# Optimization experiments

Measured on AMD Instinct MI355X. Metric: run time of the kernel, lower is better.

The kernel has to match this reference:

```python
import math
import jax, jax.numpy as jnp
import numpy as np

B, S, D, H = 2, 2048, 1024, 16
DK = D // H


def setup_inputs() -> dict:
    key = jax.random.key(0)
    ks = jax.random.split(key, 12)
    scale = 1.0 / math.sqrt(D)
    inp = {
        "q": jax.random.normal(ks[0], (B, S, D), jnp.float32),
        "k": jax.random.normal(ks[1], (B, S, D), jnp.float32),
        "v": jax.random.normal(ks[2], (B, S, D), jnp.float32),
        # causal mask, broadcast over batch and heads (mask==0 -> -inf)
        "mask": jnp.tril(jnp.ones((S, S), jnp.int32))[None, None, :, :],
        "Wq": jax.random.normal(ks[3], (D, D), jnp.float32) * scale,
        "bq": jnp.zeros((D,), jnp.float32),
        "Wk": jax.random.normal(ks[4], (D, D), jnp.float32) * scale,
        "bk": jnp.zeros((D,), jnp.float32),
        "Wv": jax.random.normal(ks[5], (D, D), jnp.float32) * scale,
        "bv": jnp.zeros((D,), jnp.float32),
        "Wo": jax.random.normal(ks[6], (D, D), jnp.float32) * scale,
        "bo": jnp.zeros((D,), jnp.float32),
    }
    return inp


def reference(q, k, v, mask, Wq, bq, Wk, bk, Wv, bv, Wo, bo):
    def proj(x, W, b):
        # [B,S,D] -> [B,H,S,DK]
        return (x @ W + b).reshape(B, -1, H, DK).transpose(0, 2, 1, 3)

    Q = proj(q, Wq, bq)
    K = proj(k, Wk, bk)
    V = proj(v, Wv, bv)
    scores = jnp.einsum("bhqd,bhkd->bhqk", Q, K) / math.sqrt(DK)  # [B,H,S,S]
    scores = jnp.where(mask == 0, -jnp.inf, scores)
    attn = jax.nn.softmax(scores, axis=-1)  # dropout p=0.0 -> identity
    ctx = jnp.einsum("bhqk,bhkd->bhqd", attn, V)
    ctx = ctx.transpose(0, 2, 1, 3).reshape(B, -1, D)  # [B,S,D]
    return ctx @ Wo + bo
```

## Files before the change

kernel.cpp:

```cpp
#include <hip/hip_runtime.h>
#include <stdint.h>

#define BB 2
#define SS 2048
#define DD 1024
#define HH 16
#define DK 64

#define QSCALE 0.1803368801111204f
#define NEGS -1.0e30f

typedef short s16x8 __attribute__((ext_vector_type(8)));
typedef float f32x4 __attribute__((ext_vector_type(4)));
typedef unsigned short u16x4 __attribute__((ext_vector_type(4)));
typedef unsigned int u32x4 __attribute__((ext_vector_type(4)));

static __device__ __forceinline__ unsigned short f2bf(float f) {
  unsigned int u = __builtin_bit_cast(unsigned int, f);
  u = (u + 0x7fffu + ((u >> 16) & 1u)) >> 16;
  return (unsigned short)u;
}

static __device__ __forceinline__ unsigned int cvtpk(float lo, float hi) {
  unsigned int r;
  asm("v_cvt_pk_bf16_f32 %0, %1, %2" : "=v"(r) : "v"(lo), "v"(hi));
  return r;
}

static __device__ __forceinline__ f32x4 mfma16(s16x8 a, s16x8 b, f32x4 c) {
  return __builtin_amdgcn_mfma_f32_16x16x32_bf16(a, b, c, 0, 0, 0);
}

static __device__ __forceinline__ void gload_lds16(const void* g, void* l) {
  __builtin_amdgcn_global_load_lds(
      (const __attribute__((address_space(1))) unsigned int*)g,
      (__attribute__((address_space(3))) unsigned int*)l, 16, 0, 0);
}

__global__ __launch_bounds__(256) void cvt3_kernel(const float* __restrict__ q,
                                                   const float* __restrict__ k,
                                                   const float* __restrict__ v,
                                                   unsigned short* __restrict__ qb,
                                                   unsigned short* __restrict__ kb,
                                                   unsigned short* __restrict__ vb) {
  int sel = blockIdx.y;
  const float* in = (sel == 0) ? q : ((sel == 1) ? k : v);
  unsigned short* out = (sel == 0) ? qb : ((sel == 1) ? kb : vb);
  int i = blockIdx.x * 256 + threadIdx.x;
  f32x4 vv = ((const f32x4*)in)[i];
  u16x4 o;
  o.x = f2bf(vv.x); o.y = f2bf(vv.y); o.z = f2bf(vv.z); o.w = f2bf(vv.w);
  ((u16x4*)out)[i] = o;
}

__global__ __launch_bounds__(256) void transpose_w4_kernel(const float* __restrict__ Wq,
                                                           const float* __restrict__ Wk,
                                                           const float* __restrict__ Wv,
                                                           const float* __restrict__ Wo,
                                                           unsigned short* __restrict__ WTbase) {
  __shared__ float t[32][33];
  int z = blockIdx.z;
  const float* W = (z == 0) ? Wq : ((z == 1) ? Wk : ((z == 2) ? Wv : Wo));
  float scale = (z == 0) ? QSCALE : 1.0f;
  unsigned short* WT = WTbase + (size_t)z * DD * DD;
  int n0 = blockIdx.x * 32, k0 = blockIdx.y * 32;
  int tx = threadIdx.x, ty = threadIdx.y;
  for (int i = 0; i < 4; ++i)
    t[ty + 8 * i][tx] = W[(size_t)(k0 + ty + 8 * i) * DD + n0 + tx];
  __syncthreads();
  for (int i = 0; i < 4; ++i)
    WT[(size_t)(n0 + ty + 8 * i) * DD + k0 + tx] = f2bf(t[tx][ty + 8 * i] * scale);
}

__global__ __launch_bounds__(256) void transpose_v_kernel(const unsigned short* __restrict__ V,
                                                          unsigned short* __restrict__ VT) {
  __shared__ unsigned short t[32][33];
  int s0 = blockIdx.x * 32, d0 = blockIdx.y * 32, bh = blockIdx.z;
  int tx = threadIdx.x, ty = threadIdx.y;
  const unsigned short* Vb = V + (size_t)bh * SS * DK;
  unsigned short* Tb = VT + (size_t)bh * DK * SS;
  for (int i = 0; i < 4; ++i)
    t[ty + 8 * i][tx] = Vb[(size_t)(s0 + ty + 8 * i) * DK + d0 + tx];
  __syncthreads();
  for (int i = 0; i < 4; ++i)
    Tb[(size_t)(d0 + ty + 8 * i) * SS + s0 + tx] = t[tx][ty + 8 * i];
}

__global__ __launch_bounds__(256) void gemm_qkv_kernel(
    const unsigned short* __restrict__ qb, const unsigned short* __restrict__ kb,
    const unsigned short* __restrict__ vb, const unsigned short* __restrict__ WTbase,
    const float* __restrict__ bq, const float* __restrict__ bk,
    const float* __restrict__ bv, unsigned short* __restrict__ Qh,
    unsigned short* __restrict__ Kh, unsigned short* __restrict__ Vh) {
  const int K = DD;
  __shared__ __align__(16) unsigned short Alds[128 * 32];
  __shared__ __align__(16) unsigned short Blds[128 * 32];
  int tid = threadIdx.x;
  int lane = tid & 63, wave = tid >> 6;
  int g = lane >> 4, r16 = lane & 15;
  int seg = blockIdx.y >> 5;
  int m0 = (blockIdx.y & 31) * 128, n0 = blockIdx.x * 128;
  int wm = (wave >> 1) * 64, wn = (wave & 1) * 64;

  const unsigned short* A = (seg == 0) ? qb : ((seg == 1) ? kb : vb);
  const unsigned short* BT = WTbase + (size_t)seg * DD * DD;
  const float* bias = (seg == 0) ? bq : ((seg == 1) ? bk : bv);
  unsigned short* outh = (seg == 0) ? Qh : ((seg == 1) ? Kh : Vh);
  float bsc = (seg == 0) ? QSCALE : 1.0f;

  f32x4 acc[4][4] = {};

  int c0 = tid, c1 = tid + 256;
  int arow0 = c0 >> 2, arow1 = c1 >> 2;
  int as0 = (c0 & 3) ^ ((arow0 >> 1) & 3);
  int as1 = (c1 & 3) ^ ((arow1 >> 1) & 3);

  for (int k0 = 0; k0 < K; k0 += 32) {
    __syncthreads();
    gload_lds16((const char*)(A + (size_t)(m0 + arow0) * K + k0) + as0 * 16,
                (char*)Alds + wave * 1024);
    gload_lds16((const char*)(A + (size_t)(m0 + arow1) * K + k0) + as1 * 16,
                (char*)Alds + wave * 1024 + 4096);
    gload_lds16((const char*)(BT + (size_t)(n0 + arow0) * K + k0) + as0 * 16,
                (char*)Blds + wave * 1024);
    gload_lds16((const char*)(BT + (size_t)(n0 + arow1) * K + k0) + as1 * 16,
                (char*)Blds + wave * 1024 + 4096);
    __syncthreads();

    s16x8 af[4], bfr[4];
#pragma unroll
    for (int mt = 0; mt < 4; ++mt) {
      int row = wm + mt * 16 + r16;
      int ch = g ^ ((row >> 1) & 3);
      af[mt] = *(const s16x8*)((const char*)Alds + row * 64 + ch * 16);
    }
#pragma unroll
    for (int nt = 0; nt < 4; ++nt) {
      int row = wn + nt * 16 + r16;
      int ch = g ^ ((row >> 1) & 3);
      bfr[nt] = *(const s16x8*)((const char*)Blds + row * 64 + ch * 16);
    }
#pragma unroll
    for (int mt = 0; mt < 4; ++mt)
#pragma unroll
      for (int nt = 0; nt < 4; ++nt)
        acc[mt][nt] = mfma16(af[mt], bfr[nt], acc[mt][nt]);
  }

#pragma unroll
  for (int nt = 0; nt < 4; ++nt) {
    int col = n0 + wn + nt * 16 + r16;
    int h = col >> 6, dk = col & (DK - 1);
    float bvv = bias[col] * bsc;
#pragma unroll
    for (int mt = 0; mt < 4; ++mt) {
#pragma unroll
      for (int rr = 0; rr < 4; ++rr) {
        int rowg = m0 + wm + mt * 16 + g * 4 + rr;
        int bb = rowg >> 11, s = rowg & (SS - 1);
        float val = acc[mt][nt][rr] + bvv;
        outh[(((size_t)bb * HH + h) * SS + s) * DK + dk] = f2bf(val);
      }
    }
  }
}

__global__ __launch_bounds__(256) void gemm_out_kernel(const unsigned short* __restrict__ A,
                                                       const unsigned short* __restrict__ BT,
                                                       const float* __restrict__ bias,
                                                       float* __restrict__ out) {
  const int K = DD;
  __shared__ __align__(16) unsigned short Alds[128 * 32];
  __shared__ __align__(16) unsigned short Blds[64 * 32];
  int tid = threadIdx.x;
  int lane = tid & 63, wave = tid >> 6;
  int g = lane >> 4, r16 = lane & 15;
  int m0 = blockIdx.y * 128, n0 = blockIdx.x * 64;
  int wm = (wave >> 1) * 64, wn = (wave & 1) * 32;

  f32x4 acc[4][2] = {};

  int c0 = tid, c1 = tid + 256;
  int arow0 = c0 >> 2, arow1 = c1 >> 2;
  int as0 = (c0 & 3) ^ ((arow0 >> 1) & 3);
  int as1 = (c1 & 3) ^ ((arow1 >> 1) & 3);

  for (int k0 = 0; k0 < K; k0 += 32) {
    __syncthreads();
    gload_lds16((const char*)(A + (size_t)(m0 + arow0) * K + k0) + as0 * 16,
                (char*)Alds + wave * 1024);
    gload_lds16((const char*)(A + (size_t)(m0 + arow1) * K + k0) + as1 * 16,
                (char*)Alds + wave * 1024 + 4096);
    gload_lds16((const char*)(BT + (size_t)(n0 + arow0) * K + k0) + as0 * 16,
                (char*)Blds + wave * 1024);
    __syncthreads();

    s16x8 af[4], bfr[2];
#pragma unroll
    for (int mt = 0; mt < 4; ++mt) {
      int row = wm + mt * 16 + r16;
      int ch = g ^ ((row >> 1) & 3);
      af[mt] = *(const s16x8*)((const char*)Alds + row * 64 + ch * 16);
    }
#pragma unroll
    for (int nt = 0; nt < 2; ++nt) {
      int row = wn + nt * 16 + r16;
      int ch = g ^ ((row >> 1) & 3);
      bfr[nt] = *(const s16x8*)((const char*)Blds + row * 64 + ch * 16);
    }
#pragma unroll
    for (int mt = 0; mt < 4; ++mt)
#pragma unroll
      for (int nt = 0; nt < 2; ++nt)
        acc[mt][nt] = mfma16(af[mt], bfr[nt], acc[mt][nt]);
  }

#pragma unroll
  for (int nt = 0; nt < 2; ++nt) {
    int col = n0 + wn + nt * 16 + r16;
    float bvv = bias[col];
#pragma unroll
    for (int mt = 0; mt < 4; ++mt) {
#pragma unroll
      for (int rr = 0; rr < 4; ++rr) {
        int rowg = m0 + wm + mt * 16 + g * 4 + rr;
        out[(size_t)rowg * DD + col] = acc[mt][nt][rr] + bvv;
      }
    }
  }
}

__global__ __launch_bounds__(256) void attn_kernel(const unsigned short* __restrict__ Qh,
                                                   const unsigned short* __restrict__ Kh,
                                                   const unsigned short* __restrict__ VhT,
                                                   unsigned short* __restrict__ ctx) {
  __shared__ __align__(16) unsigned short Klds[2][64 * 64];
  __shared__ __align__(16) unsigned short Vlds[2][64 * 64];

  int tid = threadIdx.x;
  int lane = tid & 63, wave = tid >> 6;
  int g = lane >> 4, r16 = lane & 15;
  int pid = blockIdx.x;
  int bh = blockIdx.y;

  const int NTQ = SS / 64;
  int q0A = pid * 64, q0B = (NTQ - 1 - pid) * 64;
  int tilesA = pid + 1, tilesB = NTQ - pid;

  const unsigned short* Qb = Qh + (size_t)bh * SS * DK;
  const char* Kb = (const char*)(Kh + (size_t)bh * SS * DK);
  const char* Vb = (const char*)(VhT + (size_t)bh * DK * SS);

  int a_ = r16 >> 2, b_ = r16 & 3;
  int rbase = 8 * a_ + b_;
  int sk = b_ + 4 * (a_ & 1);

  int c0 = tid, c1 = tid + 256;
  int row0 = c0 >> 3, row1 = c1 >> 3;
  int skst0 = ((row0 & 3) | (((row0 >> 3) & 1) << 2));
  int skst1 = ((row1 & 3) | (((row1 >> 3) & 1) << 2));
  int kc0 = (c0 & 7) ^ skst0, kc1 = (c1 & 7) ^ skst1;
  int vc0 = (c0 & 7) ^ (row0 & 7), vc1 = (c1 & 7) ^ (row1 & 7);

#define STAGE_KV(buf, kv0)                                                   \
  do {                                                                       \
    gload_lds16(Kb + ((size_t)((kv0) + row0) * 128) + kc0 * 16,              \
                (char*)Klds[buf] + wave * 1024);                             \
    gload_lds16(Kb + ((size_t)((kv0) + row1) * 128) + kc1 * 16,              \
                (char*)Klds[buf] + wave * 1024 + 4096);                      \
    gload_lds16(Vb + ((size_t)row0 * SS + (kv0)) * 2 + vc0 * 16,             \
                (char*)Vlds[buf] + wave * 1024);                             \
    gload_lds16(Vb + ((size_t)row1 * SS + (kv0)) * 2 + vc1 * 16,             \
                (char*)Vlds[buf] + wave * 1024 + 4096);                      \
  } while (0)

  int b = bh >> 4, h = bh & (HH - 1);

  STAGE_KV(0, 0);
  int cur = 0;

  for (int seg = 0; seg < 2; ++seg) {
    int q0 = seg ? q0B : q0A;
    int ntiles = seg ? tilesB : tilesA;
    int qw0 = q0 + wave * 16;

    s16x8 aq[2];
#pragma unroll
    for (int kc = 0; kc < 2; ++kc)
      aq[kc] = *(const s16x8*)(Qb + (size_t)(qw0 + r16) * DK + kc * 32 + g * 8);

    f32x4 accd[4] = {};
    float mrow = -INFINITY, lrow = 0.0f;

    for (int t = 0; t < ntiles; ++t) {
      int kv0 = t * 64;
      __syncthreads();
      bool more = (t + 1 < ntiles);
      if (more || seg == 0) STAGE_KV(cur ^ 1, more ? kv0 + 64 : 0);

      const char* Kc = (const char*)Klds[cur];
      const char* Vc = (const char*)Vlds[cur];

      f32x4 sf[4] = {};
      __builtin_amdgcn_s_setprio(1);
#pragma unroll
      for (int kc = 0; kc < 2; ++kc) {
        s16x8 bk[4];
#pragma unroll
        for (int nt = 0; nt < 4; ++nt) {
          int row = rbase + 4 * (nt & 1) + 32 * (nt >> 1);
          int ch = (kc * 4 + g) ^ sk;
          bk[nt] = *(const s16x8*)(Kc + row * 128 + ch * 16);
        }
#pragma unroll
        for (int nt = 0; nt < 4; ++nt)
          sf[nt] = mfma16(bk[nt], aq[kc], sf[nt]);
      }
      __builtin_amdgcn_s_setprio(0);

      s16x8 av[2][4];
#pragma unroll
      for (int c = 0; c < 2; ++c)
#pragma unroll
        for (int dsub = 0; dsub < 4; ++dsub) {
          int row = dsub * 16 + r16;
          int ch = (c * 4 + g) ^ (row & 7);
          av[c][dsub] = *(const s16x8*)(Vc + row * 128 + ch * 16);
        }

      if (kv0 + 63 > qw0) {
        int thr = qw0 + r16 - kv0 - 8 * g;
#pragma unroll
        for (int nt = 0; nt < 4; ++nt) {
          int koff = 4 * (nt & 1) + 32 * (nt >> 1);
#pragma unroll
          for (int rr = 0; rr < 4; ++rr)
            if (koff + rr > thr) sf[nt][rr] = NEGS;
        }
      }

      float tmax = NEGS;
#pragma unroll
      for (int nt = 0; nt < 4; ++nt)
#pragma unroll
        for (int rr = 0; rr < 4; ++rr) tmax = fmaxf(tmax, sf[nt][rr]);
      tmax = fmaxf(tmax, __shfl_xor(tmax, 16));
      tmax = fmaxf(tmax, __shfl_xor(tmax, 32));

      if (!__all(tmax <= mrow)) {
        float mn = fmaxf(mrow, tmax);
        float fc = __builtin_amdgcn_exp2f(mrow - mn);
        lrow *= fc;
        mrow = mn;
#pragma unroll
        for (int dsub = 0; dsub < 4; ++dsub)
#pragma unroll
          for (int rr = 0; rr < 4; ++rr) accd[dsub][rr] *= fc;
      }

      float pf[4][4];
      float su = 0.0f;
#pragma unroll
      for (int nt = 0; nt < 4; ++nt)
#pragma unroll
        for (int rr = 0; rr < 4; ++rr) {
          float p = __builtin_amdgcn_exp2f(sf[nt][rr] - mrow);
          pf[nt][rr] = p;
          su += p;
        }
      su += __shfl_xor(su, 16);
      su += __shfl_xor(su, 32);
      lrow += su;

      unsigned int pk[2][4];
#pragma unroll
      for (int c = 0; c < 2; ++c) {
        pk[c][0] = cvtpk(pf[2 * c][0], pf[2 * c][1]);
        pk[c][1] = cvtpk(pf[2 * c][2], pf[2 * c][3]);
        pk[c][2] = cvtpk(pf[2 * c + 1][0], pf[2 * c + 1][1]);
        pk[c][3] = cvtpk(pf[2 * c + 1][2], pf[2 * c + 1][3]);
      }

      __builtin_amdgcn_s_setprio(1);
#pragma unroll
      for (int c = 0; c < 2; ++c) {
        s16x8 pb = __builtin_bit_cast(s16x8, *(u32x4*)pk[c]);
#pragma unroll
        for (int dsub = 0; dsub < 4; ++dsub)
          accd[dsub] = mfma16(av[c][dsub], pb, accd[dsub]);
      }
      __builtin_amdgcn_s_setprio(0);

      cur ^= 1;
    }

    int srow = qw0 + r16;
    float inv = 1.0f / lrow;
#pragma unroll
    for (int dsub = 0; dsub < 4; ++dsub) {
      int d0 = dsub * 16 + 4 * g;
      u16x4 o;
#pragma unroll
      for (int rr = 0; rr < 4; ++rr) o[rr] = f2bf(accd[dsub][rr] * inv);
      *(u16x4*)&ctx[(((size_t)b * SS + srow) * HH + h) * DK + d0] = o;
    }
  }
#undef STAGE_KV
}

extern "C" void kernel_launch(void* const* d_in, const int* in_sizes, int n_in,
                              void* d_out, int out_size, void* d_ws, size_t ws_size,
                              hipStream_t stream) {
  const float* q = (const float*)d_in[0];
  const float* k = (const float*)d_in[1];
  const float* v = (const float*)d_in[2];
  const float* Wq = (const float*)d_in[4];
  const float* bq = (const float*)d_in[5];
  const float* Wk = (const float*)d_in[6];
  const float* bk = (const float*)d_in[7];
  const float* Wv = (const float*)d_in[8];
  const float* bv = (const float*)d_in[9];
  const float* Wo = (const float*)d_in[10];
  const float* bo = (const float*)d_in[11];

  char* ws = (char*)d_ws;
  const size_t MB = 1ull << 20;
  unsigned short* qb = (unsigned short*)(ws + 0 * MB);
  unsigned short* kb = (unsigned short*)(ws + 8 * MB);
  unsigned short* vb = (unsigned short*)(ws + 16 * MB);
  unsigned short* WTbase = (unsigned short*)(ws + 24 * MB);
  unsigned short* WoT = (unsigned short*)(ws + 30 * MB);
  unsigned short* Qh = (unsigned short*)(ws + 32 * MB);
  unsigned short* Kh = (unsigned short*)(ws + 40 * MB);
  unsigned short* Vh = (unsigned short*)(ws + 48 * MB);
  unsigned short* VhT = (unsigned short*)(ws + 16 * MB);
  unsigned short* ctx = (unsigned short*)(ws + 0 * MB);

  const int n4 = BB * SS * DD / 4;

  cvt3_kernel<<<dim3(n4 / 256, 3), 256, 0, stream>>>(q, k, v, qb, kb, vb);

  dim3 tb(32, 8);
  transpose_w4_kernel<<<dim3(32, 32, 4), tb, 0, stream>>>(Wq, Wk, Wv, Wo, WTbase);

  gemm_qkv_kernel<<<dim3(8, 96), 256, 0, stream>>>(qb, kb, vb, WTbase,
                                                   bq, bk, bv, Qh, Kh, Vh);

  transpose_v_kernel<<<dim3(SS / 32, DK / 32, BB * HH), tb, 0, stream>>>(Vh, VhT);

  attn_kernel<<<dim3(SS / 128, BB * HH), 256, 0, stream>>>(Qh, Kh, VhT, ctx);

  gemm_out_kernel<<<dim3(16, 32), 256, 0, stream>>>(ctx, WoT, bo, (float*)d_out);
}
```

Baseline: 132.6 us.

## Triple-buffer K/V staging, merge both query segments into one loop, remap blocks

Replaces the two per-segment loops in the attention kernel with a single flattened loop over both query tiles' KV tiles, so prefetching runs continuously across the segment boundary. K/V LDS staging moves from double to triple buffering, with an explicit vmcnt wait and raw barrier so two tiles are in flight. The grid becomes 1D with a block-to-(bh,pid) remap that groups 8 heads per query-tile group, which may improve L2 locality. The cost is more LDS per block, which can lower occupancy, plus extra registers to hold the first segment's output until the end.

```diff
diff --git a/kernel.cpp b/kernel.cpp
--- a/kernel.cpp
+++ b/kernel.cpp
@@ -234,18 +234,20 @@
                                                    const unsigned short* __restrict__ Kh,
                                                    const unsigned short* __restrict__ VhT,
                                                    unsigned short* __restrict__ ctx) {
-  __shared__ __align__(16) unsigned short Klds[2][64 * 64];
-  __shared__ __align__(16) unsigned short Vlds[2][64 * 64];
+  __shared__ __align__(16) unsigned short Klds[3][64 * 64];
+  __shared__ __align__(16) unsigned short Vlds[3][64 * 64];
 
   int tid = threadIdx.x;
   int lane = tid & 63, wave = tid >> 6;
   int g = lane >> 4, r16 = lane & 15;
-  int pid = blockIdx.x;
-  int bh = blockIdx.y;
+  int bid = blockIdx.x;
+  int bh = ((bid >> 7) << 3) | (bid & 7);
+  int pid = (bid >> 3) & 15;
 
   const int NTQ = SS / 64;
   int q0A = pid * 64, q0B = (NTQ - 1 - pid) * 64;
-  int tilesA = pid + 1, tilesB = NTQ - pid;
+  int tilesA = pid + 1;
+  int NT = NTQ + 1;
 
   const unsigned short* Qb = Qh + (size_t)bh * SS * DK;
   const char* Kb = (const char*)(Kh + (size_t)bh * SS * DK);
@@ -262,6 +264,7 @@
   int kc0 = (c0 & 7) ^ skst0, kc1 = (c1 & 7) ^ skst1;
   int vc0 = (c0 & 7) ^ (row0 & 7), vc1 = (c1 & 7) ^ (row1 & 7);
 
+#define KV_OF(t) ((((t) >= tilesA) ? (t) - tilesA : (t)) * 64)
 #define STAGE_KV(buf, kv0)                                                   \
   do {                                                                       \
     gload_lds16(Kb + ((size_t)((kv0) + row0) * 128) + kc0 * 16,              \
@@ -276,136 +279,159 @@
 
   int b = bh >> 4, h = bh & (HH - 1);
 
+  int qw0 = q0A + wave * 16;
+  s16x8 aq[2];
+#pragma unroll
+  for (int kc = 0; kc < 2; ++kc)
+    aq[kc] = *(const s16x8*)(Qb + (size_t)(qw0 + r16) * DK + kc * 32 + g * 8);
+
   STAGE_KV(0, 0);
-  int cur = 0;
-
-  for (int seg = 0; seg < 2; ++seg) {
-    int q0 = seg ? q0B : q0A;
-    int ntiles = seg ? tilesB : tilesA;
-    int qw0 = q0 + wave * 16;
-
-    s16x8 aq[2];
-#pragma unroll
-    for (int kc = 0; kc < 2; ++kc)
-      aq[kc] = *(const s16x8*)(Qb + (size_t)(qw0 + r16) * DK + kc * 32 + g * 8);
-
-    f32x4 accd[4] = {};
-    float mrow = -INFINITY, lrow = 0.0f;
-
-    for (int t = 0; t < ntiles; ++t) {
-      int kv0 = t * 64;
-      __syncthreads();
-      bool more = (t + 1 < ntiles);
-      if (more || seg == 0) STAGE_KV(cur ^ 1, more ? kv0 + 64 : 0);
-
-      const char* Kc = (const char*)Klds[cur];
-      const char* Vc = (const char*)Vlds[cur];
-
-      f32x4 sf[4] = {};
-      __builtin_amdgcn_s_setprio(1);
-#pragma unroll
-      for (int kc = 0; kc < 2; ++kc) {
-        s16x8 bk[4];
-#pragma unroll
-        for (int nt = 0; nt < 4; ++nt) {
-          int row = rbase + 4 * (nt & 1) + 32 * (nt >> 1);
-          int ch = (kc * 4 + g) ^ sk;
-          bk[nt] = *(const s16x8*)(Kc + row * 128 + ch * 16);
-        }
-#pragma unroll
-        for (int nt = 0; nt < 4; ++nt)
-          sf[nt] = mfma16(bk[nt], aq[kc], sf[nt]);
-      }
-      __builtin_amdgcn_s_setprio(0);
-
-      s16x8 av[2][4];
-#pragma unroll
-      for (int c = 0; c < 2; ++c)
-#pragma unroll
-        for (int dsub = 0; dsub < 4; ++dsub) {
-          int row = dsub * 16 + r16;
-          int ch = (c * 4 + g) ^ (row & 7);
-          av[c][dsub] = *(const s16x8*)(Vc + row * 128 + ch * 16);
-        }
-
-      if (kv0 + 63 > qw0) {
-        int thr = qw0 + r16 - kv0 - 8 * g;
-#pragma unroll
-        for (int nt = 0; nt < 4; ++nt) {
-          int koff = 4 * (nt & 1) + 32 * (nt >> 1);
-#pragma unroll
-          for (int rr = 0; rr < 4; ++rr)
-            if (koff + rr > thr) sf[nt][rr] = NEGS;
-        }
-      }
-
-      float tmax = NEGS;
+  STAGE_KV(1, KV_OF(1));
+
+  f32x4 accd[4] = {};
+  float mrow = -INFINITY, lrow = 0.0f;
+  u16x4 outA[4];
+  int srowA = 0;
+
+  for (int t = 0; t < NT; ++t) {
+    if (t == tilesA) {
+      float inv = 1.0f / lrow;
+      srowA = qw0 + r16;
+#pragma unroll
+      for (int dsub = 0; dsub < 4; ++dsub)
+#pragma unroll
+        for (int rr = 0; rr < 4; ++rr) outA[dsub][rr] = f2bf(accd[dsub][rr] * inv);
+      qw0 = q0B + wave * 16;
+#pragma unroll
+      for (int kc = 0; kc < 2; ++kc)
+        aq[kc] = *(const s16x8*)(Qb + (size_t)(qw0 + r16) * DK + kc * 32 + g * 8);
+#pragma unroll
+      for (int dsub = 0; dsub < 4; ++dsub) accd[dsub] = (f32x4){0.f, 0.f, 0.f, 0.f};
+      mrow = -INFINITY;
+      lrow = 0.0f;
+    }
+
+    int kv0 = KV_OF(t);
+
+    if (t < NT - 1)
+      asm volatile("s_waitcnt vmcnt(4)" ::: "memory");
+    else
+      asm volatile("s_waitcnt vmcnt(0)" ::: "memory");
+    __builtin_amdgcn_s_barrier();
+    __builtin_amdgcn_sched_barrier(0);
+    if (t + 2 < NT) STAGE_KV((t + 2) % 3, KV_OF(t + 2));
+
+    const char* Kc = (const char*)Klds[t % 3];
+    const char* Vc = (const char*)Vlds[t % 3];
+
+    f32x4 sf[4] = {};
+    __builtin_amdgcn_s_setprio(1);
+#pragma unroll
+    for (int kc = 0; kc < 2; ++kc) {
+      s16x8 bk[4];
+#pragma unroll
+      for (int nt = 0; nt < 4; ++nt) {
+        int row = rbase + 4 * (nt & 1) + 32 * (nt >> 1);
+        int ch = (kc * 4 + g) ^ sk;
+        bk[nt] = *(const s16x8*)(Kc + row * 128 + ch * 16);
+      }
 #pragma unroll
       for (int nt = 0; nt < 4; ++nt)
-#pragma unroll
-        for (int rr = 0; rr < 4; ++rr) tmax = fmaxf(tmax, sf[nt][rr]);
-      tmax = fmaxf(tmax, __shfl_xor(tmax, 16));
-      tmax = fmaxf(tmax, __shfl_xor(tmax, 32));
-
-      if (!__all(tmax <= mrow)) {
-        float mn = fmaxf(mrow, tmax);
-        float fc = __builtin_amdgcn_exp2f(mrow - mn);
-        lrow *= fc;
-        mrow = mn;
-#pragma unroll
-        for (int dsub = 0; dsub < 4; ++dsub)
-#pragma unroll
-          for (int rr = 0; rr < 4; ++rr) accd[dsub][rr] *= fc;
-      }
-
-      float pf[4][4];
-      float su = 0.0f;
-#pragma unroll
-      for (int nt = 0; nt < 4; ++nt)
-#pragma unroll
-        for (int rr = 0; rr < 4; ++rr) {
-          float p = __builtin_amdgcn_exp2f(sf[nt][rr] - mrow);
-          pf[nt][rr] = p;
-          su += p;
-        }
-      su += __shfl_xor(su, 16);
-      su += __shfl_xor(su, 32);
-      lrow += su;
-
-      unsigned int pk[2][4];
-#pragma unroll
-      for (int c = 0; c < 2; ++c) {
-        pk[c][0] = cvtpk(pf[2 * c][0], pf[2 * c][1]);
-        pk[c][1] = cvtpk(pf[2 * c][2], pf[2 * c][3]);
-        pk[c][2] = cvtpk(pf[2 * c + 1][0], pf[2 * c + 1][1]);
-        pk[c][3] = cvtpk(pf[2 * c + 1][2], pf[2 * c + 1][3]);
-      }
-
-      __builtin_amdgcn_s_setprio(1);
-#pragma unroll
-      for (int c = 0; c < 2; ++c) {
-        s16x8 pb = __builtin_bit_cast(s16x8, *(u32x4*)pk[c]);
-#pragma unroll
-        for (int dsub = 0; dsub < 4; ++dsub)
-          accd[dsub] = mfma16(av[c][dsub], pb, accd[dsub]);
-      }
-      __builtin_amdgcn_s_setprio(0);
-
-      cur ^= 1;
-    }
-
-    int srow = qw0 + r16;
-    float inv = 1.0f / lrow;
-#pragma unroll
-    for (int dsub = 0; dsub < 4; ++dsub) {
-      int d0 = dsub * 16 + 4 * g;
-      u16x4 o;
-#pragma unroll
-      for (int rr = 0; rr < 4; ++rr) o[rr] = f2bf(accd[dsub][rr] * inv);
-      *(u16x4*)&ctx[(((size_t)b * SS + srow) * HH + h) * DK + d0] = o;
-    }
+        sf[nt] = mfma16(bk[nt], aq[kc], sf[nt]);
+    }
+    __builtin_amdgcn_s_setprio(0);
+
+    s16x8 av[2][4];
+#pragma unroll
+    for (int c = 0; c < 2; ++c)
+#pragma unroll
+      for (int dsub = 0; dsub < 4; ++dsub) {
+        int row = dsub * 16 + r16;
+        int ch = (c * 4 + g) ^ (row & 7);
+        av[c][dsub] = *(const s16x8*)(Vc + row * 128 + ch * 16);
+      }
+
+    if (kv0 + 63 > qw0) {
+      int thr = qw0 + r16 - kv0 - 8 * g;
+#pragma unroll
+      for (int nt = 0; nt < 4; ++nt) {
+        int koff = 4 * (nt & 1) + 32 * (nt >> 1);
+#pragma unroll
+        for (int rr = 0; rr < 4; ++rr)
+          if (koff + rr > thr) sf[nt][rr] = NEGS;
+      }
+    }
+
+    float tmax = NEGS;
+#pragma unroll
+    for (int nt = 0; nt < 4; ++nt)
+#pragma unroll
+      for (int rr = 0; rr < 4; ++rr) tmax = fmaxf(tmax, sf[nt][rr]);
+    tmax = fmaxf(tmax, __shfl_xor(tmax, 16));
+    tmax = fmaxf(tmax, __shfl_xor(tmax, 32));
+
+    if (!__all(tmax <= mrow)) {
+      float mn = fmaxf(mrow, tmax);
+      float fc = __builtin_amdgcn_exp2f(mrow - mn);
+      lrow *= fc;
+      mrow = mn;
+#pragma unroll
+      for (int dsub = 0; dsub < 4; ++dsub)
+#pragma unroll
+        for (int rr = 0; rr < 4; ++rr) accd[dsub][rr] *= fc;
+    }
+
+    float pf[4][4];
+    float su = 0.0f;
+#pragma unroll
+    for (int nt = 0; nt < 4; ++nt)
+#pragma unroll
+      for (int rr = 0; rr < 4; ++rr) {
+        float p = __builtin_amdgcn_exp2f(sf[nt][rr] - mrow);
+        pf[nt][rr] = p;
+        su += p;
+      }
+    su += __shfl_xor(su, 16);
+    su += __shfl_xor(su, 32);
+    lrow += su;
+
+    unsigned int pk[2][4];
+#pragma unroll
+    for (int c = 0; c < 2; ++c) {
+      pk[c][0] = cvtpk(pf[2 * c][0], pf[2 * c][1]);
+      pk[c][1] = cvtpk(pf[2 * c][2], pf[2 * c][3]);
+      pk[c][2] = cvtpk(pf[2 * c + 1][0], pf[2 * c + 1][1]);
+      pk[c][3] = cvtpk(pf[2 * c + 1][2], pf[2 * c + 1][3]);
+    }
+
+    __builtin_amdgcn_s_setprio(1);
+#pragma unroll
+    for (int c = 0; c < 2; ++c) {
+      s16x8 pb = __builtin_bit_cast(s16x8, *(u32x4*)pk[c]);
+#pragma unroll
+      for (int dsub = 0; dsub < 4; ++dsub)
+        accd[dsub] = mfma16(av[c][dsub], pb, accd[dsub]);
+    }
+    __builtin_amdgcn_s_setprio(0);
+  }
+
+#pragma unroll
+  for (int dsub = 0; dsub < 4; ++dsub) {
+    int d0 = dsub * 16 + 4 * g;
+    *(u16x4*)&ctx[(((size_t)b * SS + srowA) * HH + h) * DK + d0] = outA[dsub];
+  }
+  int srow = qw0 + r16;
+  float inv = 1.0f / lrow;
+#pragma unroll
+  for (int dsub = 0; dsub < 4; ++dsub) {
+    int d0 = dsub * 16 + 4 * g;
+    u16x4 o;
+#pragma unroll
+    for (int rr = 0; rr < 4; ++rr) o[rr] = f2bf(accd[dsub][rr] * inv);
+    *(u16x4*)&ctx[(((size_t)b * SS + srow) * HH + h) * DK + d0] = o;
   }
 #undef STAGE_KV
+#undef KV_OF
 }
 
 extern "C" void kernel_launch(void* const* d_in, const int* in_sizes, int n_in,
@@ -448,7 +474,7 @@
 
   transpose_v_kernel<<<dim3(SS / 32, DK / 32, BB * HH), tb, 0, stream>>>(Vh, VhT);
 
-  attn_kernel<<<dim3(SS / 128, BB * HH), 256, 0, stream>>>(Qh, Kh, VhT, ctx);
+  attn_kernel<<<512, 256, 0, stream>>>(Qh, Kh, VhT, ctx);
 
   gemm_out_kernel<<<dim3(16, 32), 256, 0, stream>>>(ctx, WoT, bo, (float*)d_out);
 }
```

Result: no change. 130.4 us (-1.7%).
